# Optimization experiments

Hardware: AMD Instinct MI355X
Metric: run time of the kernel (lower is better)

Reference implementation:

```python
import jax, jax.numpy as jnp
import numpy as np

L, N, B, S, H = 8, 4, 2, 4096, 256  # layers, sharers, batch, seq, hidden_dim
TAU = 0.5


def _mlp5(x, w1, b1, w2, b2):
    # x: [L,N,B,S,C], w1: [L,C,H], w2: [L,H,H] -> per-layer Linear-ReLU-Linear
    h = jax.nn.relu(jnp.einsum('lnbsc,lch->lnbsh', x, w1) + b1[:, None, None, None, :])
    return jnp.einsum('lnbsh,lhd->lnbsd', h, w2) + b2[:, None, None, None, :]


def _mlp4(x, w1, b1, w2, b2):
    # x: [L,B,S,C], w1: [L,C,H], w2: [L,H,H]
    h = jax.nn.relu(jnp.einsum('lbsc,lch->lbsh', x, w1) + b1[:, None, None, :])
    return jnp.einsum('lbsh,lhd->lbsd', h, w2) + b2[:, None, None, :]


def setup_inputs() -> dict:
    key = jax.random.key(0)
    ks = jax.random.split(key, 26)
    sc = 1.0 / np.sqrt(H)
    sc2 = 1.0 / np.sqrt(2 * H)
    d = {
        'receiver_k': jax.random.normal(ks[0], (L, B, S, H), jnp.float32),
        'receiver_v': jax.random.normal(ks[1], (L, B, S, H), jnp.float32),
        'sharer_k': jax.random.normal(ks[2], (L, N, B, S, H), jnp.float32),
        'sharer_v': jax.random.normal(ks[3], (L, N, B, S, H), jnp.float32),
        'edge_weights': jax.random.uniform(ks[4], (L, N), jnp.float32),
        'alpha': jnp.zeros((L,), jnp.float32),  # layer_gates_alpha init = zeros
        'ak_w1': jax.random.normal(ks[5], (L, H, H), jnp.float32) * sc,
        'ak_b1': jnp.zeros((L, H), jnp.float32),
        'ak_w2': jax.random.normal(ks[6], (L, H, H), jnp.float32) * sc,
        'ak_b2': jnp.zeros((L, H), jnp.float32),
        'av_w1': jax.random.normal(ks[7], (L, H, H), jnp.float32) * sc,
        'av_b1': jnp.zeros((L, H), jnp.float32),
        'av_w2': jax.random.normal(ks[8], (L, H, H), jnp.float32) * sc,
        'av_b2': jnp.zeros((L, H), jnp.float32),
        'fk_w1': jax.random.normal(ks[9], (L, 2 * H, H), jnp.float32) * sc2,
        'fk_b1': jnp.zeros((L, H), jnp.float32),
        'fk_w2': jax.random.normal(ks[10], (L, H, H), jnp.float32) * sc,
        'fk_b2': jnp.zeros((L, H), jnp.float32),
        'fv_w1': jax.random.normal(ks[11], (L, 2 * H, H), jnp.float32) * sc2,
        'fv_b1': jnp.zeros((L, H), jnp.float32),
        'fv_w2': jax.random.normal(ks[12], (L, H, H), jnp.float32) * sc,
        'fv_b2': jnp.zeros((L, H), jnp.float32),
    }
    return d


def reference(receiver_k, receiver_v, sharer_k, sharer_v, edge_weights, alpha,
              ak_w1, ak_b1, ak_w2, ak_b2, av_w1, av_b1, av_w2, av_b2,
              fk_w1, fk_b1, fk_w2, fk_b2, fv_w1, fv_b1, fv_w2, fv_b2):
    gate = jax.nn.sigmoid(alpha / TAU)[:, None, None, None]  # [L,1,1,1]
    # Align each sharer cache per layer
    aligned_k = _mlp5(sharer_k, ak_w1, ak_b1, ak_w2, ak_b2)
    aligned_v = _mlp5(sharer_v, av_w1, av_b1, av_w2, av_b2)
    # Weighted aggregation over sharers, divided by sharer count
    agg_k = jnp.einsum('ln,lnbsh->lbsh', edge_weights, aligned_k) / N
    agg_v = jnp.einsum('ln,lnbsh->lbsh', edge_weights, aligned_v) / N
    # Gated fusion with receiver cache
    delta_k = _mlp4(jnp.concatenate([receiver_k, agg_k], axis=-1), fk_w1, fk_b1, fk_w2, fk_b2)
    delta_v = _mlp4(jnp.concatenate([receiver_v, agg_v], axis=-1), fv_w1, fv_b1, fv_w2, fv_b2)
    fused_k = receiver_k + gate * delta_k
    fused_v = receiver_v + gate * delta_v
    return jnp.stack([fused_k, fused_v])  # [2,L,B,S,H]
```

## Files before the change

kernel.cpp:

```cpp
#include <hip/hip_runtime.h>


typedef unsigned int  u32;
typedef unsigned short u16;
typedef __attribute__((ext_vector_type(8))) short bf16x8;
typedef __attribute__((ext_vector_type(4))) float f32x4;

#define LL   8
#define NN   4
#define HH   256
#define RPL  8192
#define BM   64
#define ST   (BM * HH)

#define LSTRIDE 655360
#define O_AKW1 0
#define O_AKW2 65536
#define O_AVW1 131072
#define O_AVW2 196608
#define O_FKW1 262144
#define O_FKW2 393216
#define O_FVW1 458752
#define O_FVW2 589824

__device__ __forceinline__ u32 f2bf(float f) {
  u32 u = __builtin_bit_cast(u32, f);
  return (u + 0x7fffu + ((u >> 16) & 1u)) >> 16;
}
__device__ __forceinline__ float4 ldf4(const float* p) { return *(const float4*)p; }

__global__ __launch_bounds__(256) void prep_wt_k(
    const float* __restrict__ s0, const float* __restrict__ s1,
    const float* __restrict__ s2, const float* __restrict__ s3,
    const float* __restrict__ s4, const float* __restrict__ s5,
    const float* __restrict__ s6, const float* __restrict__ s7,
    u16* __restrict__ wt)
{
  __shared__ float tile[32][33];
  const int mat = blockIdx.z, l = blockIdx.y, t = blockIdx.x;
  const float* src; int off, K;
  switch (mat) {
    case 0: src = s0; off = O_AKW1; K = 256; break;
    case 1: src = s1; off = O_AKW2; K = 256; break;
    case 2: src = s2; off = O_AVW1; K = 256; break;
    case 3: src = s3; off = O_AVW2; K = 256; break;
    case 4: src = s4; off = O_FKW1; K = 512; break;
    case 5: src = s5; off = O_FKW2; K = 256; break;
    case 6: src = s6; off = O_FVW1; K = 512; break;
    default: src = s7; off = O_FVW2; K = 256; break;
  }
  const int ntk = K >> 5;
  if (t >= ntk * 8) return;
  const int tk = t % ntk, tp = t / ntk;
  src += (size_t)l * K * HH;
  u16* dst = wt + (size_t)l * LSTRIDE + off;
  #pragma unroll
  for (int i = 0; i < 4; ++i) {
    int idx = threadIdx.x + i * 256;
    int r = idx >> 5, c = idx & 31;
    tile[r][c] = src[(size_t)(tk * 32 + r) * HH + tp * 32 + c];
  }
  __syncthreads();
  const int pl = threadIdx.x >> 3, kq = threadIdx.x & 7;
  const int p = tp * 32 + pl;
  ushort4 o;
  o.x = (u16)f2bf(tile[kq * 4 + 0][pl]);
  o.y = (u16)f2bf(tile[kq * 4 + 1][pl]);
  o.z = (u16)f2bf(tile[kq * 4 + 2][pl]);
  o.w = (u16)f2bf(tile[kq * 4 + 3][pl]);
  *(ushort4*)(dst + (size_t)tk * 8192 + p * 32 + kq * 4) = o;
}

__device__ __forceinline__ void zero24(f32x4 (&a)[2][4]) {
  f32x4 z = {0.f, 0.f, 0.f, 0.f};
  #pragma unroll
  for (int i = 0; i < 2; ++i)
    #pragma unroll
    for (int j = 0; j < 4; ++j) a[i][j] = z;
}

template<bool STG>
__device__ __forceinline__ void gemm8R(
    f32x4 (&acc)[2][4], const bf16x8 (&ws)[16], const u16* __restrict__ act,
    const float* __restrict__ src, u16* __restrict__ dst,
    int tid, int lr, int g)
{
  float4 slot[4];
  if (STG) {
    #pragma unroll
    for (int c = 0; c < 4; ++c)
      slot[c] = ldf4(src + (size_t)(c * 512 + tid) * 4);
  }
  #pragma unroll
  for (int kt = 0; kt < 8; ++kt) {
    bf16x8 b[4];
    #pragma unroll
    for (int fq = 0; fq < 4; ++fq) {
      int q = fq * 16 + lr;
      int k = (kt * 32 + g * 8) ^ ((q & 7) << 3);
      b[fq] = *(const bf16x8*)(act + q * HH + k);
    }
    if (STG) {
      const int s = kt & 3;
      int idx = kt * 512 + tid;
      int q = idx >> 6, c = (idx & 63) * 4;
      const float4& v = slot[s];
      ushort4 o;
      o.x = (u16)f2bf(v.x); o.y = (u16)f2bf(v.y);
      o.z = (u16)f2bf(v.z); o.w = (u16)f2bf(v.w);
      *(ushort4*)(dst + q * HH + (c ^ ((q & 7) << 3))) = o;
      if (kt + 4 < 8)
        slot[s] = ldf4(src + (size_t)((kt + 4) * 512 + tid) * 4);
    }
    #pragma unroll
    for (int fp = 0; fp < 2; ++fp)
      #pragma unroll
      for (int fq = 0; fq < 4; ++fq)
        acc[fp][fq] = __builtin_amdgcn_mfma_f32_16x16x32_bf16(ws[kt * 2 + fp], b[fq], acc[fp][fq], 0, 0, 0);
  }
}

template<bool STG>
__device__ __forceinline__ void gemm8S(
    f32x4 (&acc)[2][4], const u16* __restrict__ wtile, const u16* __restrict__ act,
    const float* __restrict__ src, u16* __restrict__ dst,
    int tid, int w, int lr, int g)
{
  const u16* wl = wtile + (w * 32 + lr) * 32 + g * 8;
  bf16x8 a[4][2];
  #pragma unroll
  for (int c = 0; c < 3; ++c)
    #pragma unroll
    for (int fp = 0; fp < 2; ++fp)
      a[c][fp] = *(const bf16x8*)(wl + c * 8192 + fp * 512);
  __builtin_amdgcn_sched_barrier(0x38F);
  float4 slot[4];
  if (STG) {
    #pragma unroll
    for (int c = 0; c < 4; ++c)
      slot[c] = ldf4(src + (size_t)(c * 512 + tid) * 4);
  }
  #pragma unroll
  for (int kt = 0; kt < 8; ++kt) {
    const int cur = kt & 3;
    if (kt < 5) {
      #pragma unroll
      for (int fp = 0; fp < 2; ++fp)
        a[(kt + 3) & 3][fp] = *(const bf16x8*)(wl + (kt + 3) * 8192 + fp * 512);
    }
    bf16x8 b[4];
    #pragma unroll
    for (int fq = 0; fq < 4; ++fq) {
      int q = fq * 16 + lr;
      int k = (kt * 32 + g * 8) ^ ((q & 7) << 3);
      b[fq] = *(const bf16x8*)(act + q * HH + k);
    }
    if (STG) {
      const int s = kt & 3;
      int idx = kt * 512 + tid;
      int q = idx >> 6, c = (idx & 63) * 4;
      const float4& v = slot[s];
      ushort4 o;
      o.x = (u16)f2bf(v.x); o.y = (u16)f2bf(v.y);
      o.z = (u16)f2bf(v.z); o.w = (u16)f2bf(v.w);
      *(ushort4*)(dst + q * HH + (c ^ ((q & 7) << 3))) = o;
      if (kt + 4 < 8)
        slot[s] = ldf4(src + (size_t)((kt + 4) * 512 + tid) * 4);
    }
    #pragma unroll
    for (int fp = 0; fp < 2; ++fp)
      #pragma unroll
      for (int fq = 0; fq < 4; ++fq)
        acc[fp][fq] = __builtin_amdgcn_mfma_f32_16x16x32_bf16(a[cur][fp], b[fq], acc[fp][fq], 0, 0, 0);
  }
}

__device__ __forceinline__ void stageDirect(u16* dst, const float* __restrict__ src, int tid) {
  #pragma unroll
  for (int i = 0; i < 8; ++i) {
    int idx = i * 512 + tid;
    float4 v = ldf4(src + (size_t)idx * 4);
    int q = idx >> 6, c = (idx & 63) * 4;
    ushort4 o;
    o.x = (u16)f2bf(v.x); o.y = (u16)f2bf(v.y);
    o.z = (u16)f2bf(v.z); o.w = (u16)f2bf(v.w);
    *(ushort4*)(dst + q * HH + (c ^ ((q & 7) << 3))) = o;
  }
}

template<bool INIT>
__device__ __forceinline__ void hsUpd(
    float* HF, f32x4 (&acc)[2][4], const float* __restrict__ b1,
    float sn, int w, int lr, int g)
{
  #pragma unroll
  for (int fp = 0; fp < 2; ++fp) {
    int p0 = w * 32 + fp * 16 + g * 4;
    float4 bv = *(const float4*)(b1 + p0);
    #pragma unroll
    for (int fq = 0; fq < 4; ++fq) {
      int q = fq * 16 + lr;
      float* addr = HF + q * HH + (p0 ^ ((q & 7) << 3));
      float4 nv;
      nv.x = sn * fmaxf(acc[fp][fq][0] + bv.x, 0.f);
      nv.y = sn * fmaxf(acc[fp][fq][1] + bv.y, 0.f);
      nv.z = sn * fmaxf(acc[fp][fq][2] + bv.z, 0.f);
      nv.w = sn * fmaxf(acc[fp][fq][3] + bv.w, 0.f);
      if (!INIT) {
        float4 old = *(float4*)addr;
        nv.x += old.x; nv.y += old.y; nv.z += old.z; nv.w += old.w;
      }
      *(float4*)addr = nv;
    }
  }
}

__device__ __forceinline__ void convertHS(const float* __restrict__ HF, u16* dst, int tid) {
  #pragma unroll
  for (int j = 0; j < 8; ++j) {
    int idx = j * 512 + tid;
    int q = idx >> 6, c = (idx & 63) * 4;
    int sw = c ^ ((q & 7) << 3);
    float4 v = *(const float4*)(HF + q * HH + sw);
    ushort4 o;
    o.x = (u16)f2bf(v.x); o.y = (u16)f2bf(v.y);
    o.z = (u16)f2bf(v.z); o.w = (u16)f2bf(v.w);
    *(ushort4*)(dst + q * HH + sw) = o;
  }
}

__device__ __forceinline__ void epiLds(
    u16* buf, f32x4 (&acc)[2][4], const float* __restrict__ bias,
    float bscale, bool doRelu, int w, int lr, int g)
{
  #pragma unroll
  for (int fp = 0; fp < 2; ++fp) {
    int p0 = w * 32 + fp * 16 + g * 4;
    float4 bv = *(const float4*)(bias + p0);
    #pragma unroll
    for (int fq = 0; fq < 4; ++fq) {
      int q = fq * 16 + lr;
      float v0 = acc[fp][fq][0] + bscale * bv.x;
      float v1 = acc[fp][fq][1] + bscale * bv.y;
      float v2 = acc[fp][fq][2] + bscale * bv.z;
      float v3 = acc[fp][fq][3] + bscale * bv.w;
      if (doRelu) {
        v0 = fmaxf(v0, 0.f); v1 = fmaxf(v1, 0.f);
        v2 = fmaxf(v2, 0.f); v3 = fmaxf(v3, 0.f);
      }
      ushort4 o;
      o.x = (u16)f2bf(v0); o.y = (u16)f2bf(v1);
      o.z = (u16)f2bf(v2); o.w = (u16)f2bf(v3);
      *(ushort4*)(buf + q * HH + (p0 ^ ((q & 7) << 3))) = o;
    }
  }
}

__device__ __forceinline__ void epiOut(
    f32x4 (&acc)[2][4], const float* __restrict__ bias,
    const float* __restrict__ recv, float* __restrict__ outp,
    float gate, int w, int lr, int g)
{
  #pragma unroll
  for (int fp = 0; fp < 2; ++fp) {
    int p0 = w * 32 + fp * 16 + g * 4;
    float4 bv = *(const float4*)(bias + p0);
    #pragma unroll
    for (int fq = 0; fq < 4; ++fq) {
      int q = fq * 16 + lr;
      float4 rv = *(const float4*)(recv + (size_t)q * HH + p0);
      float4 ov;
      ov.x = rv.x + gate * (acc[fp][fq][0] + bv.x);
      ov.y = rv.y + gate * (acc[fp][fq][1] + bv.y);
      ov.z = rv.z + gate * (acc[fp][fq][2] + bv.z);
      ov.w = rv.w + gate * (acc[fp][fq][3] + bv.w);
      *(float4*)(outp + (size_t)q * HH + p0) = ov;
    }
  }
}

__global__ __launch_bounds__(512) void CacheFuser_73873437491748_kernel(
    const float* __restrict__ recv_k, const float* __restrict__ recv_v,
    const float* __restrict__ shar_k, const float* __restrict__ shar_v,
    const float* __restrict__ ew, const float* __restrict__ alpha,
    const float* __restrict__ ak_b1, const float* __restrict__ ak_b2,
    const float* __restrict__ av_b1, const float* __restrict__ av_b2,
    const float* __restrict__ fk_b1, const float* __restrict__ fk_b2,
    const float* __restrict__ fv_b1, const float* __restrict__ fv_b2,
    const u16* __restrict__ wt, float* __restrict__ out)
{
  __shared__ u16 XA[ST];
  __shared__ u16 XB[ST];
  __shared__ float HF[ST];

  const int bid = blockIdx.x;
  const int l = bid & 7, t = bid >> 3;
  const int tid = threadIdx.x;
  const int w = tid >> 6, lane = tid & 63, lr = lane & 15, g = lane >> 4;

  u16* F0 = (u16*)HF;
  u16* F1 = (u16*)HF + ST;

  const size_t row0 = (size_t)t * BM;
  const u16* lw = wt + (size_t)l * LSTRIDE;
  const float gate = 1.f / (1.f + __expf(-2.f * alpha[l]));
  const float* ewl = ew + l * NN;

  stageDirect(XA, shar_k + ((size_t)l * NN * RPL + row0) * HH, tid);

  #pragma unroll 1
  for (int path = 0; path < 2; ++path) {
    const float* recvB = (path ? recv_v : recv_k) + ((size_t)l * RPL + row0) * HH;
    const float* sharB = (path ? shar_v : shar_k) + ((size_t)l * NN * RPL + row0) * HH;
    const u16* W1  = lw + (path ? O_AVW1 : O_AKW1);
    const u16* W2  = lw + (path ? O_AVW2 : O_AKW2);
    const u16* FW1 = lw + (path ? O_FVW1 : O_FKW1);
    const u16* FW2 = lw + (path ? O_FVW2 : O_FKW2);
    const float* b1  = (path ? av_b1 : ak_b1) + l * HH;
    const float* b2  = (path ? av_b2 : ak_b2) + l * HH;
    const float* fb1 = (path ? fv_b1 : fk_b1) + l * HH;
    const float* fb2 = (path ? fv_b2 : fk_b2) + l * HH;
    float* outp = out + ((size_t)(path * LL + l) * RPL + row0) * HH;

    bf16x8 ws[16];
    {
      const u16* wl = W1 + (w * 32 + lr) * 32 + g * 8;
      #pragma unroll
      for (int kt = 0; kt < 8; ++kt)
        #pragma unroll
        for (int fp = 0; fp < 2; ++fp)
          ws[kt * 2 + fp] = *(const bf16x8*)(wl + kt * 8192 + fp * 512);
    }

    int cur = path;
    float sS = 0.f;

    #pragma unroll 1
    for (int n = 0; n < NN; ++n) {
      float sn = ewl[n] * 0.25f; sS += sn;
      __syncthreads();
      u16* XC = cur ? XB : XA;
      u16* XO = cur ? XA : XB;
      const float* nsrc = (n < 3) ? sharB + (size_t)(n + 1) * RPL * HH : recvB;
      f32x4 h[2][4]; zero24(h);
      gemm8R<true>(h, ws, XC, nsrc, XO, tid, lr, g);
      if (n == 0) hsUpd<true >(HF, h, b1, sn, w, lr, g);
      else        hsUpd<false>(HF, h, b1, sn, w, lr, g);
      cur ^= 1;
    }
    u16* XR = cur ? XB : XA;
    u16* XD = cur ? XA : XB;
    __syncthreads();
    convertHS(HF, XD, tid);
    __syncthreads();
    f32x4 agg[2][4]; zero24(agg);
    gemm8S<false>(agg, W2, XD, nullptr, nullptr, tid, w, lr, g);
    epiLds(F0, agg, b2, sS, false, w, lr, g);
    __syncthreads();
    f32x4 h2[2][4]; zero24(h2);
    if (path == 0) {
      gemm8S<true>(h2, FW1, XR, shar_v + ((size_t)l * NN * RPL + row0) * HH, XD,
                   tid, w, lr, g);
    } else {
      gemm8S<false>(h2, FW1, XR, nullptr, nullptr, tid, w, lr, g);
    }
    gemm8S<false>(h2, FW1 + 8 * 8192, F0, nullptr, nullptr, tid, w, lr, g);
    epiLds(F1, h2, fb1, 1.f, true, w, lr, g);
    __syncthreads();
    f32x4 dd[2][4]; zero24(dd);
    gemm8S<false>(dd, FW2, F1, nullptr, nullptr, tid, w, lr, g);
    epiOut(dd, fb2, recvB, outp, gate, w, lr, g);
    cur ^= 1;
  }
}

extern "C" void kernel_launch(void* const* d_in, const int* in_sizes, int n_in,
                              void* d_out, int out_size, void* d_ws, size_t ws_size,
                              hipStream_t stream)
{
  const float* recv_k = (const float*)d_in[0];
  const float* recv_v = (const float*)d_in[1];
  const float* shar_k = (const float*)d_in[2];
  const float* shar_v = (const float*)d_in[3];
  const float* ew     = (const float*)d_in[4];
  const float* alpha  = (const float*)d_in[5];
  const float* ak_w1 = (const float*)d_in[6];  const float* ak_b1 = (const float*)d_in[7];
  const float* ak_w2 = (const float*)d_in[8];  const float* ak_b2 = (const float*)d_in[9];
  const float* av_w1 = (const float*)d_in[10]; const float* av_b1 = (const float*)d_in[11];
  const float* av_w2 = (const float*)d_in[12]; const float* av_b2 = (const float*)d_in[13];
  const float* fk_w1 = (const float*)d_in[14]; const float* fk_b1 = (const float*)d_in[15];
  const float* fk_w2 = (const float*)d_in[16]; const float* fk_b2 = (const float*)d_in[17];
  const float* fv_w1 = (const float*)d_in[18]; const float* fv_b1 = (const float*)d_in[19];
  const float* fv_w2 = (const float*)d_in[20]; const float* fv_b2 = (const float*)d_in[21];
  u16* wtw = (u16*)d_ws;
  float* outp = (float*)d_out;

  prep_wt_k<<<dim3(128, 8, 8), dim3(256), 0, stream>>>(
      ak_w1, ak_w2, av_w1, av_w2, fk_w1, fk_w2, fv_w1, fv_w2, wtw);

  CacheFuser_73873437491748_kernel<<<dim3(1024), dim3(512), 0, stream>>>(
      recv_k, recv_v, shar_k, shar_v, ew, alpha,
      ak_b1, ak_b2, av_b1, av_b2, fk_b1, fk_b2, fv_b1, fv_b2, wtw, outp);
}
```

Measured before the change: 266.3 us.

## Accumulate hidden sum in bf16 LDS and batch next-tile staging after MFMA loop

The sharer hidden-sum accumulator moves from an fp32 shared buffer to a bf16 buffer that the second GEMM reads directly. This removes the convertHS pass and one barrier, and it halves the LDS footprint of that buffer. Prefetch of the next activation tile now issues all 8 global loads up front and writes them to LDS after the MFMA loop, instead of interleaving them with a 4-deep ring. The cost is repeated bf16 rounding while accumulating across sharers, which loses precision, and more registers held for the 8 staging slots.

```diff
diff --git a/kernel.cpp b/kernel.cpp
--- a/kernel.cpp
+++ b/kernel.cpp
@@ -26,6 +26,10 @@
 __device__ __forceinline__ u32 f2bf(float f) {
   u32 u = __builtin_bit_cast(u32, f);
   return (u + 0x7fffu + ((u >> 16) & 1u)) >> 16;
+}
+__device__ __forceinline__ float bf2f(u16 b) {
+  u32 u = ((u32)b) << 16;
+  return __builtin_bit_cast(float, u);
 }
 __device__ __forceinline__ float4 ldf4(const float* p) { return *(const float4*)p; }
 
@@ -79,16 +83,24 @@
     for (int j = 0; j < 4; ++j) a[i][j] = z;
 }
 
+__device__ __forceinline__ void stWrite(u16* dst, const float4& v, int idx) {
+  int q = idx >> 6, c = (idx & 63) * 4;
+  ushort4 o;
+  o.x = (u16)f2bf(v.x); o.y = (u16)f2bf(v.y);
+  o.z = (u16)f2bf(v.z); o.w = (u16)f2bf(v.w);
+  *(ushort4*)(dst + q * HH + (c ^ ((q & 7) << 3))) = o;
+}
+
 template<bool STG>
 __device__ __forceinline__ void gemm8R(
     f32x4 (&acc)[2][4], const bf16x8 (&ws)[16], const u16* __restrict__ act,
     const float* __restrict__ src, u16* __restrict__ dst,
     int tid, int lr, int g)
 {
-  float4 slot[4];
+  float4 slot[8];
   if (STG) {
     #pragma unroll
-    for (int c = 0; c < 4; ++c)
+    for (int c = 0; c < 8; ++c)
       slot[c] = ldf4(src + (size_t)(c * 512 + tid) * 4);
   }
   #pragma unroll
@@ -99,24 +111,17 @@
       int q = fq * 16 + lr;
       int k = (kt * 32 + g * 8) ^ ((q & 7) << 3);
       b[fq] = *(const bf16x8*)(act + q * HH + k);
-    }
-    if (STG) {
-      const int s = kt & 3;
-      int idx = kt * 512 + tid;
-      int q = idx >> 6, c = (idx & 63) * 4;
-      const float4& v = slot[s];
-      ushort4 o;
-      o.x = (u16)f2bf(v.x); o.y = (u16)f2bf(v.y);
-      o.z = (u16)f2bf(v.z); o.w = (u16)f2bf(v.w);
-      *(ushort4*)(dst + q * HH + (c ^ ((q & 7) << 3))) = o;
-      if (kt + 4 < 8)
-        slot[s] = ldf4(src + (size_t)((kt + 4) * 512 + tid) * 4);
     }
     #pragma unroll
     for (int fp = 0; fp < 2; ++fp)
       #pragma unroll
       for (int fq = 0; fq < 4; ++fq)
         acc[fp][fq] = __builtin_amdgcn_mfma_f32_16x16x32_bf16(ws[kt * 2 + fp], b[fq], acc[fp][fq], 0, 0, 0);
+  }
+  if (STG) {
+    #pragma unroll
+    for (int c = 0; c < 8; ++c)
+      stWrite(dst, slot[c], c * 512 + tid);
   }
 }
 
@@ -134,10 +139,10 @@
     for (int fp = 0; fp < 2; ++fp)
       a[c][fp] = *(const bf16x8*)(wl + c * 8192 + fp * 512);
   __builtin_amdgcn_sched_barrier(0x38F);
-  float4 slot[4];
+  float4 slot[8];
   if (STG) {
     #pragma unroll
-    for (int c = 0; c < 4; ++c)
+    for (int c = 0; c < 8; ++c)
       slot[c] = ldf4(src + (size_t)(c * 512 + tid) * 4);
   }
   #pragma unroll
@@ -155,42 +160,30 @@
       int k = (kt * 32 + g * 8) ^ ((q & 7) << 3);
       b[fq] = *(const bf16x8*)(act + q * HH + k);
     }
-    if (STG) {
-      const int s = kt & 3;
-      int idx = kt * 512 + tid;
-      int q = idx >> 6, c = (idx & 63) * 4;
-      const float4& v = slot[s];
-      ushort4 o;
-      o.x = (u16)f2bf(v.x); o.y = (u16)f2bf(v.y);
-      o.z = (u16)f2bf(v.z); o.w = (u16)f2bf(v.w);
-      *(ushort4*)(dst + q * HH + (c ^ ((q & 7) << 3))) = o;
-      if (kt + 4 < 8)
-        slot[s] = ldf4(src + (size_t)((kt + 4) * 512 + tid) * 4);
-    }
     #pragma unroll
     for (int fp = 0; fp < 2; ++fp)
       #pragma unroll
       for (int fq = 0; fq < 4; ++fq)
         acc[fp][fq] = __builtin_amdgcn_mfma_f32_16x16x32_bf16(a[cur][fp], b[fq], acc[fp][fq], 0, 0, 0);
   }
+  if (STG) {
+    #pragma unroll
+    for (int c = 0; c < 8; ++c)
+      stWrite(dst, slot[c], c * 512 + tid);
+  }
 }
 
 __device__ __forceinline__ void stageDirect(u16* dst, const float* __restrict__ src, int tid) {
   #pragma unroll
   for (int i = 0; i < 8; ++i) {
-    int idx = i * 512 + tid;
-    float4 v = ldf4(src + (size_t)idx * 4);
-    int q = idx >> 6, c = (idx & 63) * 4;
-    ushort4 o;
-    o.x = (u16)f2bf(v.x); o.y = (u16)f2bf(v.y);
-    o.z = (u16)f2bf(v.z); o.w = (u16)f2bf(v.w);
-    *(ushort4*)(dst + q * HH + (c ^ ((q & 7) << 3))) = o;
+    float4 v = ldf4(src + (size_t)(i * 512 + tid) * 4);
+    stWrite(dst, v, i * 512 + tid);
   }
 }
 
 template<bool INIT>
 __device__ __forceinline__ void hsUpd(
-    float* HF, f32x4 (&acc)[2][4], const float* __restrict__ b1,
+    u16* HS, f32x4 (&acc)[2][4], const float* __restrict__ b1,
     float sn, int w, int lr, int g)
 {
   #pragma unroll
@@ -200,32 +193,21 @@
     #pragma unroll
     for (int fq = 0; fq < 4; ++fq) {
       int q = fq * 16 + lr;
-      float* addr = HF + q * HH + (p0 ^ ((q & 7) << 3));
-      float4 nv;
-      nv.x = sn * fmaxf(acc[fp][fq][0] + bv.x, 0.f);
-      nv.y = sn * fmaxf(acc[fp][fq][1] + bv.y, 0.f);
-      nv.z = sn * fmaxf(acc[fp][fq][2] + bv.z, 0.f);
-      nv.w = sn * fmaxf(acc[fp][fq][3] + bv.w, 0.f);
+      u16* addr = HS + q * HH + (p0 ^ ((q & 7) << 3));
+      float v0 = sn * fmaxf(acc[fp][fq][0] + bv.x, 0.f);
+      float v1 = sn * fmaxf(acc[fp][fq][1] + bv.y, 0.f);
+      float v2 = sn * fmaxf(acc[fp][fq][2] + bv.z, 0.f);
+      float v3 = sn * fmaxf(acc[fp][fq][3] + bv.w, 0.f);
       if (!INIT) {
-        float4 old = *(float4*)addr;
-        nv.x += old.x; nv.y += old.y; nv.z += old.z; nv.w += old.w;
+        ushort4 old = *(ushort4*)addr;
+        v0 += bf2f(old.x); v1 += bf2f(old.y);
+        v2 += bf2f(old.z); v3 += bf2f(old.w);
       }
-      *(float4*)addr = nv;
-    }
-  }
-}
-
-__device__ __forceinline__ void convertHS(const float* __restrict__ HF, u16* dst, int tid) {
-  #pragma unroll
-  for (int j = 0; j < 8; ++j) {
-    int idx = j * 512 + tid;
-    int q = idx >> 6, c = (idx & 63) * 4;
-    int sw = c ^ ((q & 7) << 3);
-    float4 v = *(const float4*)(HF + q * HH + sw);
-    ushort4 o;
-    o.x = (u16)f2bf(v.x); o.y = (u16)f2bf(v.y);
-    o.z = (u16)f2bf(v.z); o.w = (u16)f2bf(v.w);
-    *(ushort4*)(dst + q * HH + sw) = o;
+      ushort4 o;
+      o.x = (u16)f2bf(v0); o.y = (u16)f2bf(v1);
+      o.z = (u16)f2bf(v2); o.w = (u16)f2bf(v3);
+      *(ushort4*)addr = o;
+    }
   }
 }
 
@@ -291,15 +273,13 @@
 {
   __shared__ u16 XA[ST];
   __shared__ u16 XB[ST];
-  __shared__ float HF[ST];
+  __shared__ u16 HS[ST];
+  __shared__ u16 FB[ST];
 
   const int bid = blockIdx.x;
   const int l = bid & 7, t = bid >> 3;
   const int tid = threadIdx.x;
   const int w = tid >> 6, lane = tid & 63, lr = lane & 15, g = lane >> 4;
-
-  u16* F0 = (u16*)HF;
-  u16* F1 = (u16*)HF + ST;
 
   const size_t row0 = (size_t)t * BM;
   const u16* lw = wt + (size_t)l * LSTRIDE;
@@ -344,18 +324,16 @@
       const float* nsrc = (n < 3) ? sharB + (size_t)(n + 1) * RPL * HH : recvB;
       f32x4 h[2][4]; zero24(h);
       gemm8R<true>(h, ws, XC, nsrc, XO, tid, lr, g);
-      if (n == 0) hsUpd<true >(HF, h, b1, sn, w, lr, g);
-      else        hsUpd<false>(HF, h, b1, sn, w, lr, g);
+      if (n == 0) hsUpd<true >(HS, h, b1, sn, w, lr, g);
+      else        hsUpd<false>(HS, h, b1, sn, w, lr, g);
       cur ^= 1;
     }
     u16* XR = cur ? XB : XA;
     u16* XD = cur ? XA : XB;
     __syncthreads();
-    convertHS(HF, XD, tid);
-    __syncthreads();
     f32x4 agg[2][4]; zero24(agg);
-    gemm8S<false>(agg, W2, XD, nullptr, nullptr, tid, w, lr, g);
-    epiLds(F0, agg, b2, sS, false, w, lr, g);
+    gemm8S<false>(agg, W2, HS, nullptr, nullptr, tid, w, lr, g);
+    epiLds(FB, agg, b2, sS, false, w, lr, g);
     __syncthreads();
     f32x4 h2[2][4]; zero24(h2);
     if (path == 0) {
@@ -364,11 +342,11 @@
     } else {
       gemm8S<false>(h2, FW1, XR, nullptr, nullptr, tid, w, lr, g);
     }
-    gemm8S<false>(h2, FW1 + 8 * 8192, F0, nullptr, nullptr, tid, w, lr, g);
-    epiLds(F1, h2, fb1, 1.f, true, w, lr, g);
+    gemm8S<false>(h2, FW1 + 8 * 8192, FB, nullptr, nullptr, tid, w, lr, g);
+    epiLds(HS, h2, fb1, 1.f, true, w, lr, g);
     __syncthreads();
     f32x4 dd[2][4]; zero24(dd);
-    gemm8S<false>(dd, FW2, F1, nullptr, nullptr, tid, w, lr, g);
+    gemm8S<false>(dd, FW2, HS, nullptr, nullptr, tid, w, lr, g);
     epiOut(dd, fb2, recvB, outp, gate, w, lr, g);
     cur ^= 1;
   }
```

Measured after the change: 339.8 us. +27.6%, slower.
